# Kernel optimization log

Measured on AMD Instinct MI355X. Metric: run time of the kernel, lower is better.

The kernel has to match this reference:

```python
import jax, jax.numpy as jnp
import numpy as np

G = 3          # N_discretizers
K = 128        # CodebookSize
D = 16         # patch_size * patch_size
ALPHA = 1.0    # commitment weight
BSZ, C, H, W = 128, 3, 96, 96
HID, OUT = 512, 10
MLP_IN = 16 * 20 * 20


def setup_inputs() -> dict:
    key = jax.random.key(0)
    ks = jax.random.split(key, 12)
    f32 = jnp.float32
    return {
        "x": jax.random.normal(ks[0], (BSZ, C, H, W), f32),
        "codebooks": jax.random.normal(ks[1], (G, K, D), f32) * 0.1,
        "w_conv1": jax.random.normal(ks[2], (32, C, 5, 5), f32) * 0.05,
        "b_conv1": jnp.zeros((32,), f32),
        "w_conv2": jax.random.normal(ks[3], (32, 32, 5, 5), f32) * 0.05,
        "b_conv2": jnp.zeros((32,), f32),
        "w_conv3": jax.random.normal(ks[4], (16, 32, 5, 5), f32) * 0.05,
        "b_conv3": jnp.zeros((16,), f32),
        "w_fc1": jax.random.normal(ks[5], (HID, MLP_IN), f32) * 0.02,
        "b_fc1": jnp.zeros((HID,), f32),
        "w_fc2": jax.random.normal(ks[6], (OUT, HID), f32) * 0.02,
        "b_fc2": jnp.zeros((OUT,), f32),
    }


def _conv(x, w, b):
    y = jax.lax.conv_general_dilated(
        x, w, window_strides=(1, 1), padding="VALID",
        dimension_numbers=("NCHW", "OIHW", "NCHW"))
    return y + b[None, :, None, None]


def _maxpool2(x):
    return jax.lax.reduce_window(x, -jnp.inf, jax.lax.max,
                                 (1, 1, 2, 2), (1, 1, 2, 2), "VALID")


def _quantize(xp, cb):
    # xp: [N, D] flat patches; cb: [G, K, D] codebooks (one per discretizer)
    dots = jnp.einsum("nd,gkd->gnk", xp, cb)                     # [G,N,K]
    d2 = ((xp * xp).sum(-1)[None, :, None]
          - 2.0 * dots
          + (cb * cb).sum(-1)[:, None, :])                       # sq. distances
    att = jax.nn.softmax(-d2, axis=-1)                           # [G,N,K]
    idx = jnp.argmin(d2, axis=-1)                                # [G,N]
    q = cb[jnp.arange(G)[:, None], idx]                          # [G,N,D]
    # straight-through estimator, averaged over discretizers
    st = xp[None] + jax.lax.stop_gradient(q - xp[None])
    out = st.mean(axis=0)                                        # [N,D]
    # VQ codebook loss + alpha * commitment loss
    loss = (jnp.mean((q - jax.lax.stop_gradient(xp[None])) ** 2)
            + ALPHA * jnp.mean((xp[None] - jax.lax.stop_gradient(q)) ** 2))
    return out, loss, att


def reference(x, codebooks, w_conv1, b_conv1, w_conv2, b_conv2,
              w_conv3, b_conv3, w_fc1, b_fc1, w_fc2, b_fc2):
    bsz, n_ch, h, w = x.shape
    patches = x.reshape(-1, D)                                   # [N, 16]
    qp, extra_loss, att_scores = _quantize(patches, codebooks)
    xq = qp.reshape(bsz, n_ch, h, w)
    y = jax.nn.relu(_conv(xq, w_conv1, b_conv1))
    y = jax.nn.relu(_maxpool2(_conv(y, w_conv2, b_conv2)))
    y = jax.nn.relu(_maxpool2(_conv(y, w_conv3, b_conv3)))
    y = y.reshape(bsz, -1)                                       # [B, 6400]
    y = jax.nn.relu(y @ w_fc1.T + b_fc1)
    pred = y @ w_fc2.T + b_fc2
    contrastive_loss = jnp.zeros((1,), x.dtype)
    return pred, extra_loss, att_scores, contrastive_loss
```

## Files before the change

### kernel.cpp

```cpp
#include <hip/hip_runtime.h>
#include <hip/hip_bf16.h>


#define NP 221184

typedef __attribute__((ext_vector_type(8)))  short  short8;
typedef __attribute__((ext_vector_type(16))) float  f32x16;
typedef __attribute__((ext_vector_type(4)))  float  f32x4;

__global__ __launch_bounds__(256) void quant_mfma(
    const float* __restrict__ x, const float* __restrict__ cb,
    const __hip_bfloat16* __restrict__ cbp, const float* __restrict__ cbn2,
    float* __restrict__ att, float* __restrict__ xq, float* __restrict__ lossAcc)
{
  __shared__ float stage[4][64][32];
  __shared__ float sred[4][64];
  __shared__ float mred[4][64];
  __shared__ int   ired[4][64];

  const int tid  = threadIdx.x;
  const int wv   = tid >> 6;
  const int lane = tid & 63;
  const int col  = lane & 31;
  const int hi   = lane >> 5;
  const int l7   = lane & 7;
  const int n0   = blockIdx.x * 64;
  const int n    = n0 + lane;

  const float4* xp4 = (const float4*)(x + (size_t)n*16);
  float4 xa = xp4[0], xb = xp4[1], xc = xp4[2], xd = xp4[3];
  float xv[16] = {xa.x,xa.y,xa.z,xa.w, xb.x,xb.y,xb.z,xb.w,
                  xc.x,xc.y,xc.z,xc.w, xd.x,xd.y,xd.z,xd.w};

  short8 bf0, bf1;
  {
    __attribute__((aligned(16))) __hip_bfloat16 tmp[8];
    const float* p0 = x + (size_t)(n0 + col)*16 + hi*8;
    float4 u = *(const float4*)p0, v = *(const float4*)(p0 + 4);
    tmp[0]=__float2bfloat16(u.x); tmp[1]=__float2bfloat16(u.y);
    tmp[2]=__float2bfloat16(u.z); tmp[3]=__float2bfloat16(u.w);
    tmp[4]=__float2bfloat16(v.x); tmp[5]=__float2bfloat16(v.y);
    tmp[6]=__float2bfloat16(v.z); tmp[7]=__float2bfloat16(v.w);
    bf0 = *(const short8*)tmp;
    const float* p1 = x + (size_t)(n0 + 32 + col)*16 + hi*8;
    float4 u1 = *(const float4*)p1, v1 = *(const float4*)(p1 + 4);
    tmp[0]=__float2bfloat16(u1.x); tmp[1]=__float2bfloat16(u1.y);
    tmp[2]=__float2bfloat16(u1.z); tmp[3]=__float2bfloat16(u1.w);
    tmp[4]=__float2bfloat16(v1.x); tmp[5]=__float2bfloat16(v1.y);
    tmp[6]=__float2bfloat16(v1.z); tmp[7]=__float2bfloat16(v1.w);
    bf1 = *(const short8*)tmp;
  }

  float xqacc[16];
#pragma unroll
  for (int d = 0; d < 16; ++d) xqacc[d] = 0.f;
  float lossLocal = 0.f;

#pragma unroll 1
  for (int g = 0; g < 3; ++g) {
    const float* c2g = cbn2 + g*128 + wv*32;

    short8 af = *(const short8*)(cbp + ((size_t)(g*4 + wv)*64 + lane)*8);
    f32x16 zacc;
#pragma unroll
    for (int i = 0; i < 16; ++i) zacc[i] = 0.f;
    f32x16 acc0 = __builtin_amdgcn_mfma_f32_32x32x16_bf16(af, bf0, zacc, 0, 0, 0);
    f32x16 acc1 = __builtin_amdgcn_mfma_f32_32x32x16_bf16(af, bf1, zacc, 0, 0, 0);

    float e0[16], e1[16];
    float s0 = 0.f, s1 = 0.f;
    float bm0 = 3.4e38f, bm1 = 3.4e38f;
    int   bi0 = 0, bi1 = 0;
#pragma unroll
    for (int r = 0; r < 16; ++r) {
      const int row = (r & 3) + 8*(r >> 2) + 4*hi;
      const int k   = wv*32 + row;
      float c2 = c2g[row];
      float t0 = fmaf(-2.f, acc0[r], c2);
      float t1 = fmaf(-2.f, acc1[r], c2);
      float q0 = __expf(-t0);
      float q1 = __expf(-t1);
      e0[r] = q0; e1[r] = q1;
      s0 += q0; s1 += q1;
      if (t0 < bm0 || (t0 == bm0 && k < bi0)) { bm0 = t0; bi0 = k; }
      if (t1 < bm1 || (t1 == bm1 && k < bi1)) { bm1 = t1; bi1 = k; }
    }

    s0 += __shfl_xor(s0, 32);
    s1 += __shfl_xor(s1, 32);
    {
      float om = __shfl_xor(bm0, 32); int oi = __shfl_xor(bi0, 32);
      if (om < bm0 || (om == bm0 && oi < bi0)) { bm0 = om; bi0 = oi; }
      om = __shfl_xor(bm1, 32); oi = __shfl_xor(bi1, 32);
      if (om < bm1 || (om == bm1 && oi < bi1)) { bm1 = om; bi1 = oi; }
    }
    float sM  = hi ? s1 : s0;
    float bmM = hi ? bm1 : bm0;
    int   biM = hi ? bi1 : bi0;

    __syncthreads();
    sred[wv][lane] = sM;
    mred[wv][lane] = bmM;
    ired[wv][lane] = biM;
    __syncthreads();
    float stot = (sred[0][lane] + sred[1][lane]) + (sred[2][lane] + sred[3][lane]);
    float bm = mred[0][lane]; int bi = ired[0][lane];
#pragma unroll
    for (int w = 1; w < 4; ++w) {
      float m2 = mred[w][lane];
      int   i2 = ired[w][lane];
      if (m2 < bm) { bm = m2; bi = i2; }
    }
    float invL = 1.f / stot;
    float inv0 = __shfl(invL, col);
    float inv1 = __shfl(invL, col + 32);

#pragma unroll
    for (int run = 0; run < 4; ++run) {
      const int gl = run*2 + hi;
      f32x4 v;
      v[0] = e0[run*4+0]*inv0; v[1] = e0[run*4+1]*inv0;
      v[2] = e0[run*4+2]*inv0; v[3] = e0[run*4+3]*inv0;
      *(f32x4*)&stage[wv][col][(gl ^ (col & 7)) << 2] = v;
      const int p1 = col + 32;
      f32x4 w4;
      w4[0] = e1[run*4+0]*inv1; w4[1] = e1[run*4+1]*inv1;
      w4[2] = e1[run*4+2]*inv1; w4[3] = e1[run*4+3]*inv1;
      *(f32x4*)&stage[wv][p1][(gl ^ (p1 & 7)) << 2] = w4;
    }
    __builtin_amdgcn_wave_barrier();

    {
      const int pr = lane >> 3;
      const int pg = l7 ^ pr;
      float* ab = att + ((size_t)g*NP + n0)*128 + wv*32;
#pragma unroll
      for (int i = 0; i < 8; ++i) {
        int p = pr + 8*i;
        f32x4 v = *(const f32x4*)&stage[wv][p][pg << 2];
        __builtin_nontemporal_store(v, (f32x4*)(ab + (size_t)p*128 + (l7 << 2)));
      }
    }
    __builtin_amdgcn_wave_barrier();

    if (wv == 0) {
      const float4* qr = (const float4*)(cb + g*2048 + bi*16);
      float4 q0 = qr[0], q1 = qr[1], q2 = qr[2], q3 = qr[3];
      float qv[16] = {q0.x,q0.y,q0.z,q0.w, q1.x,q1.y,q1.z,q1.w,
                      q2.x,q2.y,q2.z,q2.w, q3.x,q3.y,q3.z,q3.w};
#pragma unroll
      for (int d = 0; d < 16; ++d) {
        xqacc[d] += qv[d];
        float e = qv[d] - xv[d];
        lossLocal += e*e;
      }
    }
  }

  if (wv == 0) {
    float4* xqo = (float4*)(xq + (size_t)n*16);
    const float third = 1.f/3.f;
    xqo[0] = make_float4(xqacc[0]*third, xqacc[1]*third, xqacc[2]*third, xqacc[3]*third);
    xqo[1] = make_float4(xqacc[4]*third, xqacc[5]*third, xqacc[6]*third, xqacc[7]*third);
    xqo[2] = make_float4(xqacc[8]*third, xqacc[9]*third, xqacc[10]*third, xqacc[11]*third);
    xqo[3] = make_float4(xqacc[12]*third, xqacc[13]*third, xqacc[14]*third, xqacc[15]*third);
#pragma unroll
    for (int off = 32; off > 0; off >>= 1) lossLocal += __shfl_xor(lossLocal, off);
    if (lane == 0) atomicAdd(lossAcc, lossLocal);
  }
}

__global__ __launch_bounds__(256) void pack_w_kernel(
    const float* __restrict__ w1, const float* __restrict__ w2,
    const float* __restrict__ w3, const float* __restrict__ cb,
    __hip_bfloat16* __restrict__ p1, __hip_bfloat16* __restrict__ p2,
    __hip_bfloat16* __restrict__ p3,
    float* __restrict__ cbn2, __hip_bfloat16* __restrict__ cbp)
{
  int t = blockIdx.x*256 + threadIdx.x;
  if (t < 25600) {
    int ks = t >> 9, l = (t >> 3) & 63, j = t & 7;
    int ky = ks/10, kx = (ks%10)>>1, ih = ks & 1;
    int oc = l & 31, kh = l >> 5;
    int ic = ih*16 + kh*8 + j;
    p2[t] = __float2bfloat16(w2[((oc*32 + ic)*5 + ky)*5 + kx]);
  }
  if (t < 12800) {
    int ks = t >> 9, l = (t >> 3) & 63, j = t & 7;
    int ky = ks/5, kx = ks%5;
    int oc = l & 15, kh = l >> 4;
    int ic = kh*8 + j;
    p3[t] = __float2bfloat16(w3[((oc*32 + ic)*5 + ky)*5 + kx]);
  }
  if (t < 384) {
    float s = 0.f;
#pragma unroll
    for (int d = 0; d < 16; ++d) { float v = cb[t*16 + d]; s += v*v; }
    cbn2[t] = s;
  }
  if (t < 6144) {
    int g = t >> 11, r = t & 2047;
    int ct = r >> 9, l = (r >> 3) & 63, j = r & 7;
    int code = ct*32 + (l & 31);
    int d = (l >> 5)*8 + j;
    cbp[t] = __float2bfloat16(cb[((size_t)g*128 + code)*16 + d]);
  }
  if (t < 2560) {
    int ky = t >> 9, l = (t >> 3) & 63, j = t & 7;
    int oc = l & 31, kh = l >> 5;
    int idx = kh*8 + j;
    float v = 0.f;
    if (idx < 15) {
      int kx = idx / 3, ic = idx % 3;
      v = w1[((oc*3 + ic)*5 + ky)*5 + kx];
    }
    p1[t] = __float2bfloat16(v);
  }
}

__global__ __launch_bounds__(256) void pack_wf1(
    const float* __restrict__ wf1, __hip_bfloat16* __restrict__ p)
{
  int t = blockIdx.x*256 + threadIdx.x;
  if (t < 512*6400) {
    int nn = t / 6400, k = t % 6400;
    int c = k & 15, yx = k >> 4;
    p[t] = __float2bfloat16(wf1[(size_t)nn*6400 + c*400 + yx]);
  }
}

__global__ __launch_bounds__(512) void conv1_mfma(
    const float* __restrict__ in, const __hip_bfloat16* __restrict__ wp1,
    const float* __restrict__ bias, __hip_bfloat16* __restrict__ out)
{
  __shared__ __align__(16) float ins[3][12][36];
  __shared__ __align__(16) __hip_bfloat16 imcol[12][32][24];
  __shared__ __align__(16) __hip_bfloat16 tb[8][32][40];

  int tile = blockIdx.x;
  int tx0 = (tile % 3) * 32, ty0 = (tile / 3) * 8;
  int n = blockIdx.y;

  for (int t = threadIdx.x; t < 3*12*36; t += 512) {
    int ic = t / (12*36); int r = t % (12*36); int ry = r / 36, rx = r % 36;
    int gy = ty0 + ry, gx = tx0 + rx;
    float v = 0.f;
    if (gy < 96 && gx < 96)
      v = in[(((size_t)n*3 + ic)*96 + gy)*96 + gx];
    ins[ic][ry][rx] = v;
  }
  __syncthreads();

  for (int t = threadIdx.x; t < 12*32*15; t += 512) {
    int idx = t % 15; int p = t / 15; int x = p & 31; int r = p >> 5;
    int kx = idx / 3, ic = idx - kx*3;
    imcol[r][x][idx] = __float2bfloat16(ins[ic][r][x + kx]);
  }
  for (int t = threadIdx.x; t < 12*32; t += 512)
    imcol[t >> 5][t & 31][15] = __float2bfloat16(0.f);
  __syncthreads();

  const int wave = threadIdx.x >> 6;
  const int lane = threadIdx.x & 63;
  const int col  = lane & 31;
  const int kh   = lane >> 5;

  f32x16 acc;
#pragma unroll
  for (int i = 0; i < 16; ++i) acc[i] = 0.f;

#pragma unroll
  for (int ky = 0; ky < 5; ++ky) {
    short8 a = *(const short8*)(wp1 + ky*512 + lane*8);
    short8 b = *(const short8*)&imcol[wave + ky][col][kh*8];
    acc = __builtin_amdgcn_mfma_f32_32x32x16_bf16(a, b, acc, 0, 0, 0);
  }

#pragma unroll
  for (int run = 0; run < 4; ++run) {
    __hip_bfloat16 pv[4];
#pragma unroll
    for (int j = 0; j < 4; ++j) {
      int r = run*4 + j;
      int oc = j + 8*run + 4*kh;
      pv[j] = __float2bfloat16(fmaxf(acc[r] + bias[oc], 0.f));
    }
    *(uint2*)&tb[wave][col][8*run + 4*kh] = *(const uint2*)pv;
  }
  __syncthreads();

  for (int t = threadIdx.x; t < 1024; t += 512) {
    int w = t >> 7, rem = t & 127, px = rem >> 2, q = rem & 3;
    int gy = ty0 + w, gx = tx0 + px;
    if (gy < 92 && gx < 92) {
      *(int4*)(out + ((size_t)((n*92 + gy)*92 + gx))*32 + q*8) =
          *(const int4*)&tb[w][px][q*8];
    }
  }
}

__global__ __launch_bounds__(384) void conv2_mfma(
    const __hip_bfloat16* __restrict__ in, const __hip_bfloat16* __restrict__ wp,
    const float* __restrict__ bias, __hip_bfloat16* __restrict__ out)
{
  __shared__ __align__(16) char lds[8*100*64];

  int n = blockIdx.y, rg = blockIdx.x;
  int oy0 = rg * 4;
  int tid = threadIdx.x;

  for (int t = tid; t < 3200; t += 384) {
    int row = t / 400, rem = t % 400, px = rem >> 2, g = rem & 3;
    int4 v = make_int4(0,0,0,0);
    if (px < 92)
      v = *(const int4*)(in + (((size_t)n*92 + oy0 + row)*92 + px)*32 + g*8);
    int sb = ((row*100 + px) << 6) + ((g ^ ((px >> 1) & 3)) << 4);
    *(int4*)(lds + sb) = v;
  }
  __syncthreads();

  int wv = tid >> 6, lane = tid & 63;
  int rp = wv & 1, cg = wv >> 1;
  int col = lane & 31, khalf = lane >> 5;
  int ixb = cg*32 + col;

  f32x16 acc0, acc1;
#pragma unroll
  for (int i = 0; i < 16; ++i) { acc0[i] = 0.f; acc1[i] = 0.f; }

#pragma unroll
  for (int ks = 0; ks < 50; ++ks) {
    const int ky = ks/10, kx = (ks%10)>>1, ih = ks & 1;
    short8 av = *(const short8*)(wp + ks*512 + lane*8);
    int ix = ixb + kx;
    int g  = (ih*2 + khalf) ^ ((ix >> 1) & 3);
    {
      int row = 2*rp + 0 + ky;
      short8 bv = *(const short8*)(lds + ((row*100 + ix) << 6) + (g << 4));
      acc0 = __builtin_amdgcn_mfma_f32_32x32x16_bf16(av, bv, acc0, 0, 0, 0);
    }
    {
      int row = 2*rp + 1 + ky;
      short8 bv = *(const short8*)(lds + ((row*100 + ix) << 6) + (g << 4));
      acc1 = __builtin_amdgcn_mfma_f32_32x32x16_bf16(av, bv, acc1, 0, 0, 0);
    }
  }
  __syncthreads();

  {
#pragma unroll
    for (int rq = 0; rq < 4; ++rq) {
      __hip_bfloat16 pv[4];
#pragma unroll
      for (int rr = 0; rr < 4; ++rr) {
        int r = rq*4 + rr;
        float m = fmaxf(acc0[r], acc1[r]);
        float o = __shfl_xor(m, 1);
        float p = fmaxf(m, o);
        int oc = (r & 3) + 8*(r >> 2) + 4*khalf;
        pv[rr] = __float2bfloat16(fmaxf(p + bias[oc], 0.f));
      }
      if ((lane & 1) == 0) {
        int pl = col >> 1;
        *(uint2*)(lds + wv*1024 + pl*64 + (8*rq + 4*khalf)*2) = *(const uint2*)pv;
      }
    }
  }
  __syncthreads();

  if (tid < 384) {
    int byte = tid * 16;
    int w = byte >> 10, r = byte & 1023;
    int pl = r >> 6, ocq = (r & 63) >> 4;
    int pr = rg*2 + (w & 1);
    int pc = (w >> 1)*16 + pl;
    if (pc < 44) {
      *(int4*)(out + (((size_t)n*44 + pr)*44 + pc)*32 + ocq*8) =
          *(const int4*)(lds + byte);
    }
  }
}

__global__ __launch_bounds__(384) void conv3_mfma(
    const __hip_bfloat16* __restrict__ in, const __hip_bfloat16* __restrict__ wp,
    const float* __restrict__ bias, __hip_bfloat16* __restrict__ out)
{
  __shared__ __align__(16) char lds[8*52*64];

  int n = blockIdx.y, rg = blockIdx.x;
  int oy0 = rg * 4;
  int tid = threadIdx.x;

  for (int t = tid; t < 1664; t += 384) {
    int row = t / 208, rem = t % 208, px = rem >> 2, g = rem & 3;
    int4 v = make_int4(0,0,0,0);
    if (px < 44)
      v = *(const int4*)(in + (((size_t)n*44 + oy0 + row)*44 + px)*32 + g*8);
    int sb = ((row*52 + px) << 6) + ((g ^ ((px >> 1) & 3)) << 4);
    *(int4*)(lds + sb) = v;
  }
  __syncthreads();

  int wv = tid >> 6, lane = tid & 63;
  int rp = wv & 1, cg = wv >> 1;
  int col = lane & 15, kq = lane >> 4;
  int ixb = cg*16 + col;

  f32x4 acc0, acc1;
#pragma unroll
  for (int i = 0; i < 4; ++i) { acc0[i] = 0.f; acc1[i] = 0.f; }

#pragma unroll
  for (int ks = 0; ks < 25; ++ks) {
    const int ky = ks/5, kx = ks%5;
    short8 av = *(const short8*)(wp + ks*512 + lane*8);
    int ix = ixb + kx;
    int g  = kq ^ ((ix >> 1) & 3);
    {
      int row = 2*rp + 0 + ky;
      short8 bv = *(const short8*)(lds + ((row*52 + ix) << 6) + (g << 4));
      acc0 = __builtin_amdgcn_mfma_f32_16x16x32_bf16(av, bv, acc0, 0, 0, 0);
    }
    {
      int row = 2*rp + 1 + ky;
      short8 bv = *(const short8*)(lds + ((row*52 + ix) << 6) + (g << 4));
      acc1 = __builtin_amdgcn_mfma_f32_16x16x32_bf16(av, bv, acc1, 0, 0, 0);
    }
  }
  __syncthreads();

  {
    __hip_bfloat16 pv[4];
#pragma unroll
    for (int r = 0; r < 4; ++r) {
      float m = fmaxf(acc0[r], acc1[r]);
      float o = __shfl_xor(m, 1);
      float p = fmaxf(m, o);
      int oc = kq*4 + r;
      pv[r] = __float2bfloat16(fmaxf(p + bias[oc], 0.f));
    }
    if ((lane & 1) == 0) {
      int pl = col >> 1;
      *(uint2*)(lds + wv*256 + pl*32 + kq*8) = *(const uint2*)pv;
    }
  }
  __syncthreads();

  if (tid < 96) {
    int byte = tid * 16;
    int w = byte >> 8, r = byte & 255;
    int pl = r >> 5, half = (r & 31) >> 4;
    int pr = rg*2 + (w & 1);
    int pc = (w >> 1)*8 + pl;
    if (pc < 20) {
      *(int4*)(out + (((size_t)n*20 + pr)*20 + pc)*16 + half*8) =
          *(const int4*)(lds + byte);
    }
  }
}

__global__ __launch_bounds__(256) void fc1_partial(
    const __hip_bfloat16* __restrict__ x, const __hip_bfloat16* __restrict__ w,
    float* __restrict__ part)
{
  constexpr int KC = 6400 / 16;
  __shared__ float xl[128][16];
  __shared__ float wlds[32][17];
  int nt = blockIdx.x, ks = blockIdx.y;
  int k0 = ks * KC;
  int nl = threadIdx.x & 31;
  int mg = threadIdx.x >> 5;
  float acc[16];
#pragma unroll
  for (int j = 0; j < 16; ++j) acc[j] = 0.f;

  for (int kb = 0; kb < KC; kb += 16) {
    for (int t = threadIdx.x; t < 128*16; t += 256) {
      int m = t >> 4, kk = t & 15;
      xl[m][kk] = __bfloat162float(x[(size_t)m*6400 + k0 + kb + kk]);
    }
    for (int t = threadIdx.x; t < 32*16; t += 256) {
      int nn = t >> 4, kk = t & 15;
      wlds[nn][kk] = __bfloat162float(w[(size_t)(nt*32 + nn)*6400 + k0 + kb + kk]);
    }
    __syncthreads();
#pragma unroll
    for (int kk = 0; kk < 16; ++kk) {
      float wvv = wlds[nl][kk];
#pragma unroll
      for (int j = 0; j < 16; ++j)
        acc[j] += xl[mg + 8*j][kk] * wvv;
    }
    __syncthreads();
  }
#pragma unroll
  for (int j = 0; j < 16; ++j) {
    int m = mg + 8*j;
    part[((size_t)ks*128 + m)*512 + nt*32 + nl] = acc[j];
  }
}

__global__ __launch_bounds__(256) void fc1_reduce(
    const float* __restrict__ part, const float* __restrict__ bias,
    float* __restrict__ y4)
{
  int o = blockIdx.x*256 + threadIdx.x;
  int nn = o & 511;
  float s = 0.f;
#pragma unroll
  for (int ks = 0; ks < 16; ++ks)
    s += part[(size_t)ks*65536 + o];
  y4[o] = fmaxf(s + bias[nn], 0.f);
}

__global__ __launch_bounds__(256) void fc2_kernel(
    const float* __restrict__ y4, const float* __restrict__ w2,
    const float* __restrict__ b2, float* __restrict__ pred)
{
  int o = blockIdx.x*256 + threadIdx.x;
  if (o >= 1280) return;
  int m = o / 10, c = o % 10;
  float s = 0.f;
  const float* yr = y4 + (size_t)m*512;
  const float* wr = w2 + (size_t)c*512;
#pragma unroll 8
  for (int k = 0; k < 512; ++k) s += yr[k]*wr[k];
  pred[o] = s + b2[c];
}

__global__ void finalize_kernel(const float* __restrict__ lossAcc,
                                float* __restrict__ out)
{
  out[1280] = 2.f * (*lossAcc) / 10616832.f;
  out[84935937] = 0.f;
}

extern "C" void kernel_launch(void* const* d_in, const int* in_sizes, int n_in,
                              void* d_out, int out_size, void* d_ws, size_t ws_size,
                              hipStream_t stream)
{
  const float* x   = (const float*)d_in[0];
  const float* cb  = (const float*)d_in[1];
  const float* w1  = (const float*)d_in[2];
  const float* b1  = (const float*)d_in[3];
  const float* w2  = (const float*)d_in[4];
  const float* b2  = (const float*)d_in[5];
  const float* w3  = (const float*)d_in[6];
  const float* b3  = (const float*)d_in[7];
  const float* wf1 = (const float*)d_in[8];
  const float* bf1 = (const float*)d_in[9];
  const float* wf2 = (const float*)d_in[10];
  const float* bf2 = (const float*)d_in[11];

  float* out = (float*)d_out;
  char*  ws  = (char*)d_ws;

  float*          xq   = (float*)         (ws + 0);
  __hip_bfloat16* y1   = (__hip_bfloat16*)(ws + 14155776);
  __hip_bfloat16* y2   = (__hip_bfloat16*)(ws + 83492864);
  __hip_bfloat16* y3   = (__hip_bfloat16*)(ws + 99352576);
  float*          part = (float*)         (ws + 104267776);
  __hip_bfloat16* cbp  = (__hip_bfloat16*)(ws + 104267776);
  __hip_bfloat16* wp1  = (__hip_bfloat16*)(ws + 104284160);
  float*          y4   = (float*)         (ws + 108462080);
  __hip_bfloat16* wp2  = (__hip_bfloat16*)(ws + 108724224);
  __hip_bfloat16* wp3  = (__hip_bfloat16*)(ws + 108775424);
  float*          cbn2 = (float*)         (ws + 108801024);
  float*          loss = (float*)         (ws + 108802560);
  __hip_bfloat16* wf1p = (__hip_bfloat16*)(ws + 108802624);

  hipMemsetAsync(loss, 0, sizeof(float), stream);

  pack_w_kernel<<<100, 256, 0, stream>>>(w1, w2, w3, cb, wp1, wp2, wp3, cbn2, cbp);
  pack_wf1<<<12800, 256, 0, stream>>>(wf1, wf1p);

  quant_mfma<<<3456, 256, 0, stream>>>(x, cb, cbp, cbn2, out + 1281, xq, loss);

  conv1_mfma<<<dim3(36, 128), 512, 0, stream>>>(xq, wp1, b1, y1);
  conv2_mfma<<<dim3(22, 128), 384, 0, stream>>>(y1, wp2, b2, y2);
  conv3_mfma<<<dim3(10, 128), 384, 0, stream>>>(y2, wp3, b3, y3);

  fc1_partial<<<dim3(16, 16), 256, 0, stream>>>(y3, wf1p, part);
  fc1_reduce<<<256, 256, 0, stream>>>(part, bf1, y4);
  fc2_kernel<<<5, 256, 0, stream>>>(y4, wf2, bf2, out);

  finalize_kernel<<<1, 1, 0, stream>>>(loss, out);
}
```

Baseline: 348.6 us.

## Give each wave full codebook over its own patches, removing block-level reductions

Measured after the change: 464.9 us. 1.33x slower.

```diff
diff --git a/kernel.cpp b/kernel.cpp
--- a/kernel.cpp
+++ b/kernel.cpp
@@ -8,15 +8,52 @@
 typedef __attribute__((ext_vector_type(16))) float  f32x16;
 typedef __attribute__((ext_vector_type(4)))  float  f32x4;
 
-__global__ __launch_bounds__(256) void quant_mfma(
+#define QCHUNK(C, A)                                                          \
+  {                                                                           \
+    short8 af = *(const short8*)(cbp + ((size_t)(g*4 + (C))*64 + lane)*8);    \
+    f32x16 z;                                                                 \
+    _Pragma("unroll")                                                         \
+    for (int i = 0; i < 16; ++i) z[i] = 0.f;                                  \
+    A = __builtin_amdgcn_mfma_f32_32x32x16_bf16(af, bf, z, 0, 0, 0);          \
+    _Pragma("unroll")                                                         \
+    for (int r = 0; r < 16; ++r) {                                            \
+      const int row = (r & 3) + 8*(r >> 2) + 4*hi;                            \
+      const int k   = (C)*32 + row;                                           \
+      float t = fmaf(-2.f, A[r], c2g[(C)*32 + row]);                          \
+      float e = __expf(-t);                                                   \
+      A[r] = e; s += e;                                                       \
+      if (t < bm || (t == bm && k < bi)) { bm = t; bi = k; }                  \
+    }                                                                         \
+  }
+
+#define QSTORE(C, A)                                                          \
+  {                                                                           \
+    _Pragma("unroll")                                                         \
+    for (int run = 0; run < 4; ++run) {                                       \
+      f32x4 v;                                                                \
+      v[0] = A[run*4+0]*inv; v[1] = A[run*4+1]*inv;                           \
+      v[2] = A[run*4+2]*inv; v[3] = A[run*4+3]*inv;                           \
+      *(f32x4*)&stage[wv][col][((run*2 + hi) ^ (col & 7)) << 2] = v;          \
+    }                                                                         \
+    __builtin_amdgcn_wave_barrier();                                          \
+    {                                                                         \
+      float* ab = att + ((size_t)g*NP + n0w)*128 + (C)*32;                    \
+      _Pragma("unroll")                                                       \
+      for (int i = 0; i < 4; ++i) {                                           \
+        int p = (lane >> 3) + 8*i;                                            \
+        f32x4 v = *(const f32x4*)&stage[wv][p][pg << 2];                      \
+        __builtin_nontemporal_store(v, (f32x4*)(ab + (size_t)p*128 + l7*4));  \
+      }                                                                       \
+    }                                                                         \
+    __builtin_amdgcn_wave_barrier();                                          \
+  }
+
+__global__ __launch_bounds__(256) void quant_v9(
     const float* __restrict__ x, const float* __restrict__ cb,
     const __hip_bfloat16* __restrict__ cbp, const float* __restrict__ cbn2,
     float* __restrict__ att, float* __restrict__ xq, float* __restrict__ lossAcc)
 {
-  __shared__ float stage[4][64][32];
-  __shared__ float sred[4][64];
-  __shared__ float mred[4][64];
-  __shared__ int   ired[4][64];
+  __shared__ float stage[4][32][32];
 
   const int tid  = threadIdx.x;
   const int wv   = tid >> 6;
@@ -24,31 +61,25 @@
   const int col  = lane & 31;
   const int hi   = lane >> 5;
   const int l7   = lane & 7;
-  const int n0   = blockIdx.x * 64;
-  const int n    = n0 + lane;
-
-  const float4* xp4 = (const float4*)(x + (size_t)n*16);
+  const int pg   = l7 ^ (lane >> 3);
+  const int n0w  = (blockIdx.x*4 + wv) * 32;
+  const int np   = n0w + col;
+
+  const float4* xp4 = (const float4*)(x + (size_t)np*16);
   float4 xa = xp4[0], xb = xp4[1], xc = xp4[2], xd = xp4[3];
   float xv[16] = {xa.x,xa.y,xa.z,xa.w, xb.x,xb.y,xb.z,xb.w,
                   xc.x,xc.y,xc.z,xc.w, xd.x,xd.y,xd.z,xd.w};
 
-  short8 bf0, bf1;
+  short8 bf;
   {
     __attribute__((aligned(16))) __hip_bfloat16 tmp[8];
-    const float* p0 = x + (size_t)(n0 + col)*16 + hi*8;
+    const float* p0 = x + (size_t)np*16 + hi*8;
     float4 u = *(const float4*)p0, v = *(const float4*)(p0 + 4);
     tmp[0]=__float2bfloat16(u.x); tmp[1]=__float2bfloat16(u.y);
     tmp[2]=__float2bfloat16(u.z); tmp[3]=__float2bfloat16(u.w);
     tmp[4]=__float2bfloat16(v.x); tmp[5]=__float2bfloat16(v.y);
     tmp[6]=__float2bfloat16(v.z); tmp[7]=__float2bfloat16(v.w);
-    bf0 = *(const short8*)tmp;
-    const float* p1 = x + (size_t)(n0 + 32 + col)*16 + hi*8;
-    float4 u1 = *(const float4*)p1, v1 = *(const float4*)(p1 + 4);
-    tmp[0]=__float2bfloat16(u1.x); tmp[1]=__float2bfloat16(u1.y);
-    tmp[2]=__float2bfloat16(u1.z); tmp[3]=__float2bfloat16(u1.w);
-    tmp[4]=__float2bfloat16(v1.x); tmp[5]=__float2bfloat16(v1.y);
-    tmp[6]=__float2bfloat16(v1.z); tmp[7]=__float2bfloat16(v1.w);
-    bf1 = *(const short8*)tmp;
+    bf = *(const short8*)tmp;
   }
 
   float xqacc[16];
@@ -58,92 +89,29 @@
 
 #pragma unroll 1
   for (int g = 0; g < 3; ++g) {
-    const float* c2g = cbn2 + g*128 + wv*32;
-
-    short8 af = *(const short8*)(cbp + ((size_t)(g*4 + wv)*64 + lane)*8);
-    f32x16 zacc;
-#pragma unroll
-    for (int i = 0; i < 16; ++i) zacc[i] = 0.f;
-    f32x16 acc0 = __builtin_amdgcn_mfma_f32_32x32x16_bf16(af, bf0, zacc, 0, 0, 0);
-    f32x16 acc1 = __builtin_amdgcn_mfma_f32_32x32x16_bf16(af, bf1, zacc, 0, 0, 0);
-
-    float e0[16], e1[16];
-    float s0 = 0.f, s1 = 0.f;
-    float bm0 = 3.4e38f, bm1 = 3.4e38f;
-    int   bi0 = 0, bi1 = 0;
-#pragma unroll
-    for (int r = 0; r < 16; ++r) {
-      const int row = (r & 3) + 8*(r >> 2) + 4*hi;
-      const int k   = wv*32 + row;
-      float c2 = c2g[row];
-      float t0 = fmaf(-2.f, acc0[r], c2);
-      float t1 = fmaf(-2.f, acc1[r], c2);
-      float q0 = __expf(-t0);
-      float q1 = __expf(-t1);
-      e0[r] = q0; e1[r] = q1;
-      s0 += q0; s1 += q1;
-      if (t0 < bm0 || (t0 == bm0 && k < bi0)) { bm0 = t0; bi0 = k; }
-      if (t1 < bm1 || (t1 == bm1 && k < bi1)) { bm1 = t1; bi1 = k; }
-    }
-
-    s0 += __shfl_xor(s0, 32);
-    s1 += __shfl_xor(s1, 32);
+    const float* c2g = cbn2 + g*128;
+
+    float s = 0.f;
+    float bm = 3.4e38f; int bi = 0;
+    f32x16 a0, a1, a2, a3;
+    QCHUNK(0, a0)
+    QCHUNK(1, a1)
+    QCHUNK(2, a2)
+    QCHUNK(3, a3)
+
+    s += __shfl_xor(s, 32);
     {
-      float om = __shfl_xor(bm0, 32); int oi = __shfl_xor(bi0, 32);
-      if (om < bm0 || (om == bm0 && oi < bi0)) { bm0 = om; bi0 = oi; }
-      om = __shfl_xor(bm1, 32); oi = __shfl_xor(bi1, 32);
-      if (om < bm1 || (om == bm1 && oi < bi1)) { bm1 = om; bi1 = oi; }
-    }
-    float sM  = hi ? s1 : s0;
-    float bmM = hi ? bm1 : bm0;
-    int   biM = hi ? bi1 : bi0;
-
-    __syncthreads();
-    sred[wv][lane] = sM;
-    mred[wv][lane] = bmM;
-    ired[wv][lane] = biM;
-    __syncthreads();
-    float stot = (sred[0][lane] + sred[1][lane]) + (sred[2][lane] + sred[3][lane]);
-    float bm = mred[0][lane]; int bi = ired[0][lane];
-#pragma unroll
-    for (int w = 1; w < 4; ++w) {
-      float m2 = mred[w][lane];
-      int   i2 = ired[w][lane];
-      if (m2 < bm) { bm = m2; bi = i2; }
-    }
-    float invL = 1.f / stot;
-    float inv0 = __shfl(invL, col);
-    float inv1 = __shfl(invL, col + 32);
-
-#pragma unroll
-    for (int run = 0; run < 4; ++run) {
-      const int gl = run*2 + hi;
-      f32x4 v;
-      v[0] = e0[run*4+0]*inv0; v[1] = e0[run*4+1]*inv0;
-      v[2] = e0[run*4+2]*inv0; v[3] = e0[run*4+3]*inv0;
-      *(f32x4*)&stage[wv][col][(gl ^ (col & 7)) << 2] = v;
-      const int p1 = col + 32;
-      f32x4 w4;
-      w4[0] = e1[run*4+0]*inv1; w4[1] = e1[run*4+1]*inv1;
-      w4[2] = e1[run*4+2]*inv1; w4[3] = e1[run*4+3]*inv1;
-      *(f32x4*)&stage[wv][p1][(gl ^ (p1 & 7)) << 2] = w4;
-    }
-    __builtin_amdgcn_wave_barrier();
-
-    {
-      const int pr = lane >> 3;
-      const int pg = l7 ^ pr;
-      float* ab = att + ((size_t)g*NP + n0)*128 + wv*32;
-#pragma unroll
-      for (int i = 0; i < 8; ++i) {
-        int p = pr + 8*i;
-        f32x4 v = *(const f32x4*)&stage[wv][p][pg << 2];
-        __builtin_nontemporal_store(v, (f32x4*)(ab + (size_t)p*128 + (l7 << 2)));
-      }
-    }
-    __builtin_amdgcn_wave_barrier();
-
-    if (wv == 0) {
+      float om = __shfl_xor(bm, 32); int oi = __shfl_xor(bi, 32);
+      if (om < bm || (om == bm && oi < bi)) { bm = om; bi = oi; }
+    }
+    const float inv = 1.f / s;
+
+    QSTORE(0, a0)
+    QSTORE(1, a1)
+    QSTORE(2, a2)
+    QSTORE(3, a3)
+
+    if (hi == 0) {
       const float4* qr = (const float4*)(cb + g*2048 + bi*16);
       float4 q0 = qr[0], q1 = qr[1], q2 = qr[2], q3 = qr[3];
       float qv[16] = {q0.x,q0.y,q0.z,q0.w, q1.x,q1.y,q1.z,q1.w,
@@ -157,17 +125,17 @@
     }
   }
 
-  if (wv == 0) {
-    float4* xqo = (float4*)(xq + (size_t)n*16);
+  if (hi == 0) {
+    float4* xqo = (float4*)(xq + (size_t)np*16);
     const float third = 1.f/3.f;
     xqo[0] = make_float4(xqacc[0]*third, xqacc[1]*third, xqacc[2]*third, xqacc[3]*third);
     xqo[1] = make_float4(xqacc[4]*third, xqacc[5]*third, xqacc[6]*third, xqacc[7]*third);
     xqo[2] = make_float4(xqacc[8]*third, xqacc[9]*third, xqacc[10]*third, xqacc[11]*third);
     xqo[3] = make_float4(xqacc[12]*third, xqacc[13]*third, xqacc[14]*third, xqacc[15]*third);
-#pragma unroll
-    for (int off = 32; off > 0; off >>= 1) lossLocal += __shfl_xor(lossLocal, off);
-    if (lane == 0) atomicAdd(lossAcc, lossLocal);
-  }
+  }
+#pragma unroll
+  for (int off = 32; off > 0; off >>= 1) lossLocal += __shfl_xor(lossLocal, off);
+  if (lane == 0) atomicAdd(lossAcc, lossLocal);
 }
 
 __global__ __launch_bounds__(256) void pack_w_kernel(
@@ -574,7 +542,7 @@
   pack_w_kernel<<<100, 256, 0, stream>>>(w1, w2, w3, cb, wp1, wp2, wp3, cbn2, cbp);
   pack_wf1<<<12800, 256, 0, stream>>>(wf1, wf1p);
 
-  quant_mfma<<<3456, 256, 0, stream>>>(x, cb, cbp, cbn2, out + 1281, xq, loss);
+  quant_v9<<<1728, 256, 0, stream>>>(x, cb, cbp, cbn2, out + 1281, xq, loss);
 
   conv1_mfma<<<dim3(36, 128), 512, 0, stream>>>(xq, wp1, b1, y1);
   conv2_mfma<<<dim3(22, 128), 384, 0, stream>>>(y1, wp2, b2, y2);
```
